# Kernel tuning notes

Measured on AMD Instinct MI355X. Metric: run time of the kernel, lower is better.

The kernel has to match this reference:

```python
import jax, jax.numpy as jnp
import numpy as np


def _ln(x, g, b, eps=1e-5):
    m = x.mean(-1, keepdims=True)
    v = x.var(-1, keepdims=True)
    return (x - m) / jnp.sqrt(v + eps) * g + b


def _causal_linear_attn(q, k, v, eps=1e-3):
    # q, k, v: (b, h, n, d). Matches lucidrains causal_linear_attn with bucket_size=1:
    # q -> softmax over feature dim, k -> exp, inclusive cumsum of k and k(outer)v over n.
    dh = q.shape[-1]
    q = jax.nn.softmax(q, axis=-1) * (dh ** -0.5)
    k = jnp.exp(k)
    k_cum = jnp.cumsum(k, axis=2)                                  # (b,h,n,d)
    ctx = jnp.cumsum(k[..., :, None] * v[..., None, :], axis=2)    # (b,h,n,d,d) running sum of k_i v_i^T
    d_inv = 1.0 / jnp.clip(jnp.einsum('bhnd,bhnd->bhn', k_cum, q), eps, None)
    return jnp.einsum('bhnd,bhnde->bhne', q, ctx) * d_inv[..., None]


def reference(x, ln1_g, ln1_b, Wq, Wk, Wv, Wo, bo, ln2_g, ln2_b, W1, b1, W2, b2, n_heads):
    depth = Wq.shape[0]
    B, N, D = x.shape
    H = int(n_heads)
    dh = D // H
    for i in range(depth):
        # --- pre-norm linear self-attention block ---
        xn = _ln(x, ln1_g[i], ln1_b[i])
        q = (xn @ Wq[i]).reshape(B, N, H, dh).transpose(0, 2, 1, 3)
        k = (xn @ Wk[i]).reshape(B, N, H, dh).transpose(0, 2, 1, 3)
        v = (xn @ Wv[i]).reshape(B, N, H, dh).transpose(0, 2, 1, 3)
        a = _causal_linear_attn(q, k, v)
        a = a.transpose(0, 2, 1, 3).reshape(B, N, D)
        x = x + a @ Wo[i] + bo[i]
        # --- pre-norm feed-forward block (mult=4, exact GELU) ---
        xn = _ln(x, ln2_g[i], ln2_b[i])
        x = x + jax.nn.gelu(xn @ W1[i] + b1[i], approximate=False) @ W2[i] + b2[i]
    return x


def setup_inputs() -> dict:
    key = jax.random.key(0)
    ks = jax.random.split(key, 8)
    B, N, D, H, depth = 2, 2048, 1024, 16, 2
    FF = 4 * D
    s = D ** -0.5
    x = jax.random.normal(ks[0], (B, N, D), dtype=jnp.float32)
    Wq = jax.random.normal(ks[1], (depth, D, D), dtype=jnp.float32) * s
    Wk = jax.random.normal(ks[2], (depth, D, D), dtype=jnp.float32) * s
    Wv = jax.random.normal(ks[3], (depth, D, D), dtype=jnp.float32) * s
    Wo = jax.random.normal(ks[4], (depth, D, D), dtype=jnp.float32) * s
    W1 = jax.random.normal(ks[5], (depth, D, FF), dtype=jnp.float32) * s
    W2 = jax.random.normal(ks[6], (depth, FF, D), dtype=jnp.float32) * (FF ** -0.5)
    return dict(
        x=x,
        ln1_g=jnp.ones((depth, D), jnp.float32), ln1_b=jnp.zeros((depth, D), jnp.float32),
        Wq=Wq, Wk=Wk, Wv=Wv, Wo=Wo, bo=jnp.zeros((depth, D), jnp.float32),
        ln2_g=jnp.ones((depth, D), jnp.float32), ln2_b=jnp.zeros((depth, D), jnp.float32),
        W1=W1, b1=jnp.zeros((depth, FF), jnp.float32),
        W2=W2, b2=jnp.zeros((depth, D), jnp.float32),
        n_heads=H,
    )
```

## Files before the change

kernel.cpp:

```cpp
#include <hip/hip_runtime.h>
#include <cmath>

#define BB 2
#define SEQ 2048
#define DIM 1024
#define NH 16
#define DH 64
#define DEPTH 2
#define FFD 4096
#define CHK 64
#define NCHK (SEQ/CHK)
#define ROWS (BB*SEQ)
#define QKP (3*DIM)

typedef __bf16 bf16x8 __attribute__((ext_vector_type(8)));
typedef __bf16 bf16x4 __attribute__((ext_vector_type(4)));
typedef float  f32x4  __attribute__((ext_vector_type(4)));

#define AS1 __attribute__((address_space(1)))
#define AS3 __attribute__((address_space(3)))
#define FENCE() asm volatile("" ::: "memory")

__device__ __forceinline__ float gelu_fast(float x) {
    float x3 = x * x * x;
    float y = 1.5957691216057308f * (x + 0.044715f * x3);
    return x * __builtin_amdgcn_rcpf(1.0f + __expf(-y));
}

__device__ __forceinline__ int swz128(int row, int col) {
    return row * 64 + (col ^ ((row & 7) << 3));
}

__device__ __forceinline__ void swz_tile(int bid, int NX, int NY, int& tx, int& ty) {
    int NB = NX * NY;
    int q = NB >> 3, r = NB & 7;
    int xcd = bid & 7, seq = bid >> 3;
    int start = (xcd < r) ? xcd * (q + 1) : r * (q + 1) + (xcd - r) * q;
    int wgid = start + seq;
    int g = 0, rem = wgid;
    int gw = (NX < 4) ? NX : 4;
    while (rem >= gw * NY) {
        rem -= gw * NY; g++;
        int left = NX - 4 * g;
        gw = left < 4 ? left : 4;
    }
    ty = rem / gw;
    tx = 4 * g + rem % gw;
}

__global__ __launch_bounds__(256) void ln_kernel(
    const float* __restrict__ x, const float* __restrict__ g,
    const float* __restrict__ b, __bf16* __restrict__ out)
{
    int row = blockIdx.x;
    const float4* xr = (const float4*)(x + (size_t)row * DIM);
    int t = threadIdx.x;
    float4 v = xr[t];
    float s  = v.x + v.y + v.z + v.w;
    float ss = v.x*v.x + v.y*v.y + v.z*v.z + v.w*v.w;
    #pragma unroll
    for (int off = 32; off > 0; off >>= 1) {
        s  += __shfl_down(s, off);
        ss += __shfl_down(ss, off);
    }
    __shared__ float wsum[4], wsq[4], stats[2];
    int wid = t >> 6, lane = t & 63;
    if (lane == 0) { wsum[wid] = s; wsq[wid] = ss; }
    __syncthreads();
    if (t == 0) {
        float S  = wsum[0] + wsum[1] + wsum[2] + wsum[3];
        float SS = wsq[0] + wsq[1] + wsq[2] + wsq[3];
        float mean = S * (1.0f / DIM);
        float var  = SS * (1.0f / DIM) - mean * mean;
        stats[0] = mean;
        stats[1] = rsqrtf(var + 1e-5f);
    }
    __syncthreads();
    float mean = stats[0], rstd = stats[1];
    float4 gv = ((const float4*)g)[t];
    float4 bv = ((const float4*)b)[t];
    bf16x4 o;
    o[0] = (__bf16)((v.x - mean) * rstd * gv.x + bv.x);
    o[1] = (__bf16)((v.y - mean) * rstd * gv.y + bv.y);
    o[2] = (__bf16)((v.z - mean) * rstd * gv.z + bv.z);
    o[3] = (__bf16)((v.w - mean) * rstd * gv.w + bv.w);
    *(bf16x4*)(out + (size_t)row * DIM + t * 4) = o;
}

__global__ __launch_bounds__(256) void transpose_all(
    const float* __restrict__ wq, const float* __restrict__ wk,
    const float* __restrict__ wv, const float* __restrict__ wo,
    const float* __restrict__ w1, const float* __restrict__ w2,
    __bf16* __restrict__ wqkt, __bf16* __restrict__ wot,
    __bf16* __restrict__ w1t, __bf16* __restrict__ w2t)
{
    int id = blockIdx.x;
    const float* W; __bf16* Wt; int K, N, txt, tyt;
    if (id < 4096) {
        int seg = id >> 10, r = id & 1023;
        K = DIM; N = DIM;
        txt = r & 31; tyt = r >> 5;
        W  = seg == 0 ? wq : seg == 1 ? wk : seg == 2 ? wv : wo;
        Wt = seg < 3 ? wqkt + (size_t)seg * DIM * DIM : wot;
    } else if (id < 8192) {
        int r = id - 4096;
        K = DIM; N = FFD;
        txt = r & 127; tyt = r >> 7;
        W = w1; Wt = w1t;
    } else {
        int r = id - 8192;
        K = FFD; N = DIM;
        txt = r & 31; tyt = r >> 5;
        W = w2; Wt = w2t;
    }
    __shared__ float tile[32][33];
    int bx = txt * 32, by = tyt * 32;
    int tx = threadIdx.x & 31, ty = threadIdx.x >> 5;
    #pragma unroll
    for (int i = 0; i < 32; i += 8)
        tile[ty + i][tx] = W[(size_t)(by + ty + i) * N + bx + tx];
    __syncthreads();
    #pragma unroll
    for (int i = 0; i < 32; i += 8)
        Wt[(size_t)(bx + ty + i) * K + by + tx] = (__bf16)tile[tx][ty + i];
}

__global__ __launch_bounds__(256) void transpose_v(
    const __bf16* __restrict__ qkv, __bf16* __restrict__ vT)
{
    __shared__ __bf16 tile[64 * 64];
    int bx = blockIdx.x;
    int by = blockIdx.y;
    int t = threadIdx.x;
    int r0 = t >> 3, sl = t & 7;
    #pragma unroll
    for (int i = 0; i < 2; i++) {
        int row = i * 32 + r0;
        bf16x8 d = *(const bf16x8*)(qkv + (size_t)(bx * 64 + row) * QKP + 2 * DIM + by * 64 + sl * 8);
        *(bf16x8*)&tile[row * 64 + ((sl ^ (row & 7)) << 3)] = d;
    }
    __syncthreads();
    #pragma unroll
    for (int i = 0; i < 2; i++) {
        int d = i * 32 + r0;
        int rbase = sl * 8;
        bf16x8 o;
        #pragma unroll
        for (int j = 0; j < 8; j++) {
            int rr = rbase + j;
            o[j] = tile[rr * 64 + (((((d >> 3)) ^ (rr & 7)) << 3) | (d & 7))];
        }
        *(bf16x8*)(vT + (size_t)(by * 64 + d) * ROWS + bx * 64 + rbase) = o;
    }
}

#define TBM 256
#define TBK 64
template<int MODE, int OUTBF, int NBF>
__global__ __launch_bounds__(512) void gemm256(
    const __bf16* __restrict__ A, const __bf16* __restrict__ Bt,
    void* __restrict__ Cv, const float* __restrict__ bias,
    const float* __restrict__ res, int M, int N, int K, int Kp,
    int NXT, int NYT, int NS)
{
    constexpr int ASZ = TBM * TBK;
    constexpr int BSZ = NBF * 64 * TBK;
    __shared__ __bf16 lds[2 * (ASZ + BSZ)];
    int nb = NXT * NYT;
    int sk = blockIdx.x / nb;
    int tx, ty;
    swz_tile(blockIdx.x % nb, NXT, NYT, tx, ty);
    if (NS > 1) {
        A  += (size_t)sk * K;
        Bt += (size_t)sk * K;
        Cv = (void*)((char*)Cv + (size_t)sk * M * N * (OUTBF ? 2 : 4));
    }
    const int bm = ty * TBM, bn = tx * (NBF * 64);
    const int t = threadIdx.x;
    const int l = t & 63, w = t >> 6;
    const int wm = w >> 2, wn = w & 3;
    const int lm = l & 15, lk = l >> 4;

    f32x4 acc[8][NBF] = {};
    const int nt = K / TBK;
    const int NIT = nt / 2;

    auto Aoff = [&](int bf) { return bf * (ASZ + BSZ); };
    auto Boff = [&](int bf) { return bf * (ASZ + BSZ) + ASZ; };

    const int s7 = lm & 7;
    const int c0 = (lk ^ s7) << 3;
    const int c1 = ((4 ^ lk) ^ s7) << 3;
    const __bf16* pA[2][2] = {
        { &lds[Aoff(0) + (wm * 128 + lm) * 64 + c0], &lds[Aoff(0) + (wm * 128 + lm) * 64 + c1] },
        { &lds[Aoff(1) + (wm * 128 + lm) * 64 + c0], &lds[Aoff(1) + (wm * 128 + lm) * 64 + c1] } };
    const __bf16* pB[2][2] = {
        { &lds[Boff(0) + (wn * (NBF * 16) + lm) * 64 + c0], &lds[Boff(0) + (wn * (NBF * 16) + lm) * 64 + c1] },
        { &lds[Boff(1) + (wn * (NBF * 16) + lm) * 64 + c0], &lds[Boff(1) + (wn * (NBF * 16) + lm) * 64 + c1] } };

    const int srow0 = t >> 3;
    const int scol0 = ((t & 7) ^ (srow0 & 7)) * 8;
    const __bf16* gAb = A + (size_t)(bm + srow0) * Kp + scol0;
    const __bf16* gBb = Bt + (size_t)(bn + srow0) * Kp + scol0;
    const int ldsw = w * 512;

    auto STAGEA = [&](int bf, int kt) {
        #pragma unroll
        for (int u = 0; u < 4; u++)
            __builtin_amdgcn_global_load_lds(
                (const AS1 void*)(gAb + (size_t)(u * 64) * Kp + kt * 64),
                (AS3 void*)(&lds[Aoff(bf) + u * 4096 + ldsw]), 16, 0, 0);
    };
    auto STAGEB = [&](int bf, int kt) {
        #pragma unroll
        for (int u = 0; u < NBF; u++)
            __builtin_amdgcn_global_load_lds(
                (const AS1 void*)(gBb + (size_t)(u * 64) * Kp + kt * 64),
                (AS3 void*)(&lds[Boff(bf) + u * 4096 + ldsw]), 16, 0, 0);
    };
    auto VMCNT_N = [&]() {
        if constexpr (NBF == 4) asm volatile("s_waitcnt vmcnt(4)" ::: "memory");
        else if constexpr (NBF == 3) asm volatile("s_waitcnt vmcnt(3)" ::: "memory");
        else asm volatile("s_waitcnt vmcnt(2)" ::: "memory");
    };
    auto LDA = [&](int bf, int g, bf16x8* af) {
        #pragma unroll
        for (int j = 0; j < 4; j++) {
            af[j * 2 + 0] = *(const bf16x8*)(pA[bf][0] + (g * 4 + j) * 1024);
            af[j * 2 + 1] = *(const bf16x8*)(pA[bf][1] + (g * 4 + j) * 1024);
        }
    };
    auto LDB = [&](int bf, bf16x8* bfv) {
        #pragma unroll
        for (int n = 0; n < NBF; n++) {
            bfv[n * 2 + 0] = *(const bf16x8*)(pB[bf][0] + n * 1024);
            bfv[n * 2 + 1] = *(const bf16x8*)(pB[bf][1] + n * 1024);
        }
    };
    auto MM2 = [&](int g, bf16x8* af, bf16x8* bfv) {
        __builtin_amdgcn_s_setprio(1);
        #pragma unroll
        for (int j = 0; j < 4; j++)
            #pragma unroll
            for (int n = 0; n < NBF; n++)
                #pragma unroll
                for (int kk = 0; kk < 2; kk++)
                    acc[g * 4 + j][n] = __builtin_amdgcn_mfma_f32_16x16x32_bf16(
                        af[j * 2 + kk], bfv[n * 2 + kk], acc[g * 4 + j][n], 0, 0, 0);
        __builtin_amdgcn_s_setprio(0);
    };

    STAGEA(0, 0); STAGEB(0, 0); STAGEB(1, 1);
    VMCNT_N();
    __builtin_amdgcn_s_barrier();

    bf16x8 aF[8], aFn[8], bF[2 * NBF];
    for (int it = 0; it < NIT; it++) {
        int u = 2 * it + 1, T2 = 2 * it + 2, U2 = 2 * it + 3;
        LDA(0, 0, aF); LDB(0, bF);
        STAGEA(1, u);
        FENCE(); __builtin_amdgcn_s_barrier();
        LDA(0, 1, aFn);
        MM2(0, aF, bF);
        FENCE(); __builtin_amdgcn_s_barrier();
        if (T2 < nt) {
            STAGEB(0, T2);
            VMCNT_N();
        } else {
            asm volatile("s_waitcnt vmcnt(0)" ::: "memory");
        }
        __builtin_amdgcn_s_barrier();
        MM2(1, aFn, bF);
        FENCE(); __builtin_amdgcn_s_barrier();
        LDA(1, 0, aF); LDB(1, bF);
        if (T2 < nt) STAGEA(0, T2);
        FENCE(); __builtin_amdgcn_s_barrier();
        LDA(1, 1, aFn);
        MM2(0, aF, bF);
        FENCE(); __builtin_amdgcn_s_barrier();
        if (U2 < nt) {
            STAGEB(1, U2);
            VMCNT_N();
        } else {
            asm volatile("s_waitcnt vmcnt(0)" ::: "memory");
        }
        __builtin_amdgcn_s_barrier();
        MM2(1, aFn, bF);
        FENCE(); __builtin_amdgcn_s_barrier();
    }

    #pragma unroll
    for (int m = 0; m < 8; m++) {
        #pragma unroll
        for (int n = 0; n < NBF; n++) {
            int col = bn + wn * (NBF * 16) + n * 16 + lm;
            #pragma unroll
            for (int r = 0; r < 4; r++) {
                int row = bm + wm * 128 + m * 16 + lk * 4 + r;
                float v = acc[m][n][r];
                if (MODE == 1) v += res[(size_t)row * N + col] + bias[col];
                if (MODE == 2) v = gelu_fast(v + bias[col]);
                if (OUTBF) ((__bf16*)Cv)[(size_t)row * N + col] = (__bf16)v;
                else       ((float*)Cv)[(size_t)row * N + col] = v;
            }
        }
    }
}

template<int DOLN>
__global__ __launch_bounds__(256) void reduce4ln(
    const __bf16* __restrict__ parts, const float* __restrict__ bias,
    float* __restrict__ x, const float* __restrict__ g,
    const float* __restrict__ b, __bf16* __restrict__ xn)
{
    const size_t PS = (size_t)ROWS * DIM;
    int row = blockIdx.x, t = threadIdx.x;
    size_t base = (size_t)row * DIM + t * 4;
    float4 xr = *(const float4*)(x + base);
    float4 bv = ((const float4*)bias)[t];
    float o0 = xr.x + bv.x, o1 = xr.y + bv.y, o2 = xr.z + bv.z, o3 = xr.w + bv.w;
    #pragma unroll
    for (int s = 0; s < 4; s++) {
        bf16x4 p = *(const bf16x4*)(parts + s * PS + base);
        o0 += (float)p[0]; o1 += (float)p[1]; o2 += (float)p[2]; o3 += (float)p[3];
    }
    float4 o = {o0, o1, o2, o3};
    *(float4*)(x + base) = o;
    if constexpr (DOLN) {
        float s  = o0 + o1 + o2 + o3;
        float ss = o0*o0 + o1*o1 + o2*o2 + o3*o3;
        #pragma unroll
        for (int off = 32; off > 0; off >>= 1) {
            s  += __shfl_down(s, off);
            ss += __shfl_down(ss, off);
        }
        __shared__ float wsum[4], wsq[4], stats[2];
        int wid = t >> 6, lane = t & 63;
        if (lane == 0) { wsum[wid] = s; wsq[wid] = ss; }
        __syncthreads();
        if (t == 0) {
            float S  = wsum[0] + wsum[1] + wsum[2] + wsum[3];
            float SS = wsq[0] + wsq[1] + wsq[2] + wsq[3];
            float mean = S * (1.0f / DIM);
            float var  = SS * (1.0f / DIM) - mean * mean;
            stats[0] = mean;
            stats[1] = rsqrtf(var + 1e-5f);
        }
        __syncthreads();
        float mean = stats[0], rstd = stats[1];
        float4 gv = ((const float4*)g)[t];
        float4 bvv = ((const float4*)b)[t];
        bf16x4 on;
        on[0] = (__bf16)((o0 - mean) * rstd * gv.x + bvv.x);
        on[1] = (__bf16)((o1 - mean) * rstd * gv.y + bvv.y);
        on[2] = (__bf16)((o2 - mean) * rstd * gv.z + bvv.z);
        on[3] = (__bf16)((o3 - mean) * rstd * gv.w + bvv.w);
        *(bf16x4*)(xn + base) = on;
    }
}

__global__ __launch_bounds__(256) void attn_local_m(
    const __bf16* __restrict__ qkv, const __bf16* __restrict__ vTg,
    float* __restrict__ KVT, float* __restrict__ Ksum)
{
    int blk = blockIdx.x;
    int c = blk % NCHK, bh = blk / NCHK;
    int b = bh / NH, h = bh % NH;
    __shared__ __bf16 ek_s[64 * 64];
    __shared__ __bf16 ekT_s[64 * 68];
    __shared__ float ksum_p[4][64];
    int t = threadIdx.x, w = t >> 6, l = t & 63;
    size_t rowbase = (size_t)(b * SEQ + c * CHK);

    {
        int m = t >> 2, dq = t & 3;
        const __bf16* kr = qkv + (rowbase + m) * QKP + DIM + h * DH + dq * 16;
        bf16x8 k0 = *(const bf16x8*)kr;
        bf16x8 k1 = *(const bf16x8*)(kr + 8);
        bf16x8 e0, e1;
        #pragma unroll
        for (int j = 0; j < 8; j++) {
            e0[j] = (__bf16)__expf((float)k0[j]);
            e1[j] = (__bf16)__expf((float)k1[j]);
        }
        *(bf16x8*)&ek_s[swz128(m, dq * 16)] = e0;
        *(bf16x8*)&ek_s[swz128(m, dq * 16 + 8)] = e1;
    }
    __syncthreads();
    {
        float kacc = 0.f;
        #pragma unroll
        for (int g = 0; g < 4; g++) {
            bf16x4 pk;
            #pragma unroll
            for (int j = 0; j < 4; j++) {
                __bf16 e = ek_s[swz128(w * 16 + g * 4 + j, l)];
                pk[j] = e;
                kacc += (float)e;
            }
            *(bf16x4*)&ekT_s[l * 68 + w * 16 + g * 4] = pk;
        }
        ksum_p[w][l] = kacc;
    }
    __syncthreads();
    f32x4 acc[4] = {};
    const __bf16* vbase = vTg + (size_t)(h * DH + w * 16 + (l & 15)) * ROWS
                        + (size_t)b * SEQ + c * CHK + (l >> 4) * 8;
    bf16x8 a0 = *(const bf16x8*)vbase;
    bf16x8 a1 = *(const bf16x8*)(vbase + 32);
    #pragma unroll
    for (int fn = 0; fn < 4; fn++) {
        int rbase = (fn * 16 + (l & 15)) * 68 + (l >> 4) * 8;
        bf16x4 b0a = *(const bf16x4*)&ekT_s[rbase];
        bf16x4 b0b = *(const bf16x4*)&ekT_s[rbase + 4];
        bf16x4 b1a = *(const bf16x4*)&ekT_s[rbase + 32];
        bf16x4 b1b = *(const bf16x4*)&ekT_s[rbase + 36];
        bf16x8 b0, b1;
        #pragma unroll
        for (int j = 0; j < 4; j++) {
            b0[j] = b0a[j]; b0[j + 4] = b0b[j];
            b1[j] = b1a[j]; b1[j + 4] = b1b[j];
        }
        acc[fn] = __builtin_amdgcn_mfma_f32_16x16x32_bf16(a0, b0, acc[fn], 0, 0, 0);
        acc[fn] = __builtin_amdgcn_mfma_f32_16x16x32_bf16(a1, b1, acc[fn], 0, 0, 0);
    }
    float* kvout = KVT + (size_t)(bh * NCHK + c) * (DH * DH);
    #pragma unroll
    for (int fn = 0; fn < 4; fn++)
        #pragma unroll
        for (int r = 0; r < 4; r++)
            kvout[(w * 16 + (l >> 4) * 4 + r) * DH + fn * 16 + (l & 15)] = acc[fn][r];
    if (t < 64) {
        float s = ksum_p[0][t] + ksum_p[1][t] + ksum_p[2][t] + ksum_p[3][t];
        Ksum[(size_t)(bh * NCHK + c) * DH + t] = s;
    }
}

__global__ __launch_bounds__(256) void attn_scan2(
    float* __restrict__ KV, float* __restrict__ Ksum)
{
    int bh = blockIdx.y;
    int bx = blockIdx.x;
    int t = threadIdx.x;
    if (bx < 16) {
        int elem = bx * 256 + t;
        float run = 0.f;
        for (int c = 0; c < NCHK; c++) {
            float* p = KV + ((size_t)(bh * NCHK + c)) * (DH * DH) + elem;
            float tmp = *p;
            *p = run;
            run += tmp;
        }
    } else if (t < DH) {
        float run = 0.f;
        for (int c = 0; c < NCHK; c++) {
            float* p = Ksum + ((size_t)(bh * NCHK + c)) * DH + t;
            float tmp = *p;
            *p = run;
            run += tmp;
        }
    }
}

__global__ __launch_bounds__(256) void attn_out_m(
    const __bf16* __restrict__ qkv, const __bf16* __restrict__ vTg,
    const float* __restrict__ KVT, const float* __restrict__ Ksum,
    __bf16* __restrict__ ag)
{
    int blk = blockIdx.x;
    int c = blk % NCHK, bh = blk / NCHK;
    int b = bh / NH, h = bh % NH;
    __shared__ __bf16 q_s[64 * 64];
    __shared__ __bf16 ek_s[64 * 64];
    __shared__ __bf16 s_s[64 * 64];
    __shared__ __bf16 kvT_s[64 * 64];
    __shared__ float denom_s[64];
    int t = threadIdx.x, w = t >> 6, l = t & 63;
    size_t rowbase = (size_t)(b * SEQ + c * CHK);

    {
        int i = t >> 2, dq = t & 3;
        const __bf16* qr = qkv + (rowbase + i) * QKP + h * DH + dq * 16;
        bf16x8 q0 = *(const bf16x8*)qr, q1 = *(const bf16x8*)(qr + 8);
        float qf[16];
        #pragma unroll
        for (int j = 0; j < 8; j++) { qf[j] = (float)q0[j]; qf[8 + j] = (float)q1[j]; }
        float mx = qf[0];
        #pragma unroll
        for (int j = 1; j < 16; j++) mx = fmaxf(mx, qf[j]);
        mx = fmaxf(mx, __shfl_xor(mx, 1));
        mx = fmaxf(mx, __shfl_xor(mx, 2));
        float ss = 0.f;
        #pragma unroll
        for (int j = 0; j < 16; j++) { qf[j] = __expf(qf[j] - mx); ss += qf[j]; }
        ss += __shfl_xor(ss, 1);
        ss += __shfl_xor(ss, 2);
        float sc = 0.125f / ss;
        bf16x8 o0, o1;
        #pragma unroll
        for (int j = 0; j < 8; j++) {
            o0[j] = (__bf16)(qf[j] * sc);
            o1[j] = (__bf16)(qf[8 + j] * sc);
        }
        *(bf16x8*)&q_s[swz128(i, dq * 16)] = o0;
        *(bf16x8*)&q_s[swz128(i, dq * 16 + 8)] = o1;
        const float* kp = Ksum + (size_t)(bh * NCHK + c) * DH + dq * 16;
        float dk = 0.f;
        #pragma unroll
        for (int j = 0; j < 16; j++) dk += (qf[j] * sc) * kp[j];
        dk += __shfl_xor(dk, 1);
        dk += __shfl_xor(dk, 2);
        if (dq == 0) denom_s[i] = dk;
    }
    {
        int m = t >> 2, dq = t & 3;
        const __bf16* kr = qkv + (rowbase + m) * QKP + DIM + h * DH + dq * 16;
        bf16x8 k0 = *(const bf16x8*)kr, k1 = *(const bf16x8*)(kr + 8);
        bf16x8 e0, e1;
        #pragma unroll
        for (int j = 0; j < 8; j++) {
            e0[j] = (__bf16)__expf((float)k0[j]);
            e1[j] = (__bf16)__expf((float)k1[j]);
        }
        *(bf16x8*)&ek_s[swz128(m, dq * 16)] = e0;
        *(bf16x8*)&ek_s[swz128(m, dq * 16 + 8)] = e1;
    }
    {
        int e = t >> 2, dq = t & 3;
        const float* kvr = KVT + (size_t)(bh * NCHK + c) * (DH * DH) + e * DH + dq * 16;
        bf16x8 o0, o1;
        #pragma unroll
        for (int j = 0; j < 8; j++) { o0[j] = (__bf16)kvr[j]; o1[j] = (__bf16)kvr[8 + j]; }
        *(bf16x8*)&kvT_s[swz128(e, dq * 16)] = o0;
        *(bf16x8*)&kvT_s[swz128(e, dq * 16 + 8)] = o1;
    }
    __syncthreads();

    bf16x8 bq0 = *(const bf16x8*)&q_s[swz128(w * 16 + (l & 15), (l >> 4) * 8)];
    bf16x8 bq1 = *(const bf16x8*)&q_s[swz128(w * 16 + (l & 15), 32 + (l >> 4) * 8)];
    int i_col = w * 16 + (l & 15);
    float dsum = 0.f;
    #pragma unroll
    for (int fm = 0; fm < 4; fm++) {
        bf16x8 ae0 = *(const bf16x8*)&ek_s[swz128(fm * 16 + (l & 15), (l >> 4) * 8)];
        bf16x8 ae1 = *(const bf16x8*)&ek_s[swz128(fm * 16 + (l & 15), 32 + (l >> 4) * 8)];
        f32x4 z = {};
        z = __builtin_amdgcn_mfma_f32_16x16x32_bf16(ae0, bq0, z, 0, 0, 0);
        z = __builtin_amdgcn_mfma_f32_16x16x32_bf16(ae1, bq1, z, 0, 0, 0);
        bf16x4 pk;
        #pragma unroll
        for (int r = 0; r < 4; r++) {
            int m = fm * 16 + (l >> 4) * 4 + r;
            float v = (m <= i_col) ? z[r] : 0.f;
            pk[r] = (__bf16)v;
            dsum += (float)pk[r];
        }
        *(bf16x4*)&s_s[swz128(i_col, fm * 16 + (l >> 4) * 4)] = pk;
    }
    dsum += __shfl_xor(dsum, 16);
    dsum += __shfl_xor(dsum, 32);
    if (l < 16) denom_s[w * 16 + l] += dsum;

    bf16x8 as0 = *(const bf16x8*)&s_s[swz128(w * 16 + (l & 15), (l >> 4) * 8)];
    bf16x8 as1 = *(const bf16x8*)&s_s[swz128(w * 16 + (l & 15), 32 + (l >> 4) * 8)];
    f32x4 oacc[4] = {};
    #pragma unroll
    for (int fn = 0; fn < 4; fn++) {
        const __bf16* vb = vTg + (size_t)(h * DH + fn * 16 + (l & 15)) * ROWS
                         + (size_t)b * SEQ + c * CHK + (l >> 4) * 8;
        bf16x8 bv0 = *(const bf16x8*)vb;
        bf16x8 bv1 = *(const bf16x8*)(vb + 32);
        bf16x8 bk0 = *(const bf16x8*)&kvT_s[swz128(fn * 16 + (l & 15), (l >> 4) * 8)];
        bf16x8 bk1 = *(const bf16x8*)&kvT_s[swz128(fn * 16 + (l & 15), 32 + (l >> 4) * 8)];
        f32x4 z = oacc[fn];
        z = __builtin_amdgcn_mfma_f32_16x16x32_bf16(as0, bv0, z, 0, 0, 0);
        z = __builtin_amdgcn_mfma_f32_16x16x32_bf16(as1, bv1, z, 0, 0, 0);
        z = __builtin_amdgcn_mfma_f32_16x16x32_bf16(bq0, bk0, z, 0, 0, 0);
        z = __builtin_amdgcn_mfma_f32_16x16x32_bf16(bq1, bk1, z, 0, 0, 0);
        oacc[fn] = z;
    }
    #pragma unroll
    for (int r = 0; r < 4; r++) {
        int i = w * 16 + (l >> 4) * 4 + r;
        float dinv = 1.0f / fmaxf(denom_s[i], 1e-3f);
        #pragma unroll
        for (int fn = 0; fn < 4; fn++)
            ag[(rowbase + i) * DIM + h * DH + fn * 16 + (l & 15)] = (__bf16)(oacc[fn][r] * dinv);
    }
}

extern "C" void kernel_launch(void* const* d_in, const int* in_sizes, int n_in,
                              void* d_out, int out_size, void* d_ws, size_t ws_size,
                              hipStream_t stream) {
    (void)in_sizes; (void)n_in; (void)out_size; (void)ws_size;
    const float* x_in  = (const float*)d_in[0];
    const float* ln1_g = (const float*)d_in[1];
    const float* ln1_b = (const float*)d_in[2];
    const float* Wq    = (const float*)d_in[3];
    const float* Wk    = (const float*)d_in[4];
    const float* Wv    = (const float*)d_in[5];
    const float* Wo    = (const float*)d_in[6];
    const float* bo    = (const float*)d_in[7];
    const float* ln2_g = (const float*)d_in[8];
    const float* ln2_b = (const float*)d_in[9];
    const float* W1    = (const float*)d_in[10];
    const float* b1    = (const float*)d_in[11];
    const float* W2    = (const float*)d_in[12];
    const float* b2    = (const float*)d_in[13];

    float* x = (float*)d_out;
    const size_t MB = 1024 * 1024;
    char* base = (char*)d_ws;

    __bf16* qkv    = (__bf16*)base;
    __bf16* partsO = (__bf16*)base;
    __bf16* h1     = (__bf16*)base;
    __bf16* vTg    = (__bf16*)(base + 24 * MB);
    __bf16* xn     = (__bf16*)(base + 32 * MB);
    __bf16* parts  = (__bf16*)(base + 32 * MB);
    __bf16* a      = (__bf16*)(base + 40 * MB);
    float*  KVT    = (float*)(base + 48 * MB);
    float*  Ks     = (float*)(base + 64 * MB);
    __bf16* wqkt   = (__bf16*)(base + 65 * MB);
    __bf16* wot    = (__bf16*)(base + 71 * MB);
    __bf16* w1t    = (__bf16*)(base + 73 * MB);
    __bf16* w2t    = (__bf16*)(base + 81 * MB);

    const size_t SZ = (size_t)ROWS * DIM;
    hipMemcpyAsync(x, x_in, SZ * sizeof(float), hipMemcpyDeviceToDevice, stream);

    dim3 gScan(17, BB * NH);
    dim3 gTv(ROWS / 64, DIM / 64);

    for (int l = 0; l < DEPTH; l++) {
        const float* wq = Wq + (size_t)l * DIM * DIM;
        const float* wk = Wk + (size_t)l * DIM * DIM;
        const float* wv = Wv + (size_t)l * DIM * DIM;
        const float* wo = Wo + (size_t)l * DIM * DIM;
        const float* w1 = W1 + (size_t)l * DIM * FFD;
        const float* w2 = W2 + (size_t)l * FFD * DIM;

        transpose_all<<<12288, 256, 0, stream>>>(wq, wk, wv, wo, w1, w2,
                                                 wqkt, wot, w1t, w2t);

        if (l == 0)
            ln_kernel<<<ROWS, 256, 0, stream>>>(x, ln1_g, ln1_b, xn);
        gemm256<0, 1, 3><<<16 * 16, 512, 0, stream>>>(xn, wqkt, qkv, nullptr, nullptr,
                                                      ROWS, QKP, DIM, DIM, 16, 16, 1);
        transpose_v<<<gTv, 256, 0, stream>>>(qkv, vTg);
        attn_local_m<<<BB * NH * NCHK, 256, 0, stream>>>(qkv, vTg, KVT, Ks);
        attn_scan2<<<gScan, 256, 0, stream>>>(KVT, Ks);
        attn_out_m<<<BB * NH * NCHK, 256, 0, stream>>>(qkv, vTg, KVT, Ks, a);
        gemm256<0, 1, 4><<<4 * 16 * 4, 512, 0, stream>>>(a, wot, partsO, nullptr, nullptr,
                                                         ROWS, DIM, DIM / 4, DIM, 4, 16, 4);
        reduce4ln<1><<<ROWS, 256, 0, stream>>>(partsO, bo + l * DIM, x,
                                               ln2_g + l * DIM, ln2_b + l * DIM, xn);

        gemm256<2, 1, 4><<<16 * 16, 512, 0, stream>>>(xn, w1t, h1, b1 + l * FFD, nullptr,
                                                      ROWS, FFD, DIM, DIM, 16, 16, 1);
        gemm256<0, 1, 4><<<4 * 16 * 4, 512, 0, stream>>>(h1, w2t, parts, nullptr, nullptr,
                                                         ROWS, DIM, FFD / 4, FFD, 4, 16, 4);
        if (l + 1 < DEPTH)
            reduce4ln<1><<<ROWS, 256, 0, stream>>>(parts, b2 + l * DIM, x,
                                                   ln1_g + (l + 1) * DIM,
                                                   ln1_b + (l + 1) * DIM, xn);
        else
            reduce4ln<0><<<ROWS, 256, 0, stream>>>(parts, b2 + l * DIM, x,
                                                   nullptr, nullptr, nullptr);
    }
}
```

Baseline: 390.8 us.

## Split GEMM mainloop into quarter-tile phases with half-staged global loads

Restructures the 256-row GEMM main loop so each k-tile is computed in four quarter phases (A half × B half), with global-to-LDS staging split into halves interleaved between phases and explicit lgkmcnt/vmcnt waits. The aim is to cut register pressure from holding full A/B fragment sets and to spread memory traffic more evenly against MFMA work. In exchange it adds roughly twice as many barriers per iteration and fragile hand-tuned vmcnt counts that could stall or race if miscounted.

```diff
diff --git a/kernel.cpp b/kernel.cpp
--- a/kernel.cpp
+++ b/kernel.cpp
@@ -20,6 +20,15 @@
 #define AS1 __attribute__((address_space(1)))
 #define AS3 __attribute__((address_space(3)))
 #define FENCE() asm volatile("" ::: "memory")
+#define LGKM0() asm volatile("s_waitcnt lgkmcnt(0)" ::: "memory")
+
+template<int N> __device__ __forceinline__ void vmcnt_wait() {
+    if constexpr (N == 0) asm volatile("s_waitcnt vmcnt(0)" ::: "memory");
+    else if constexpr (N == 3) asm volatile("s_waitcnt vmcnt(3)" ::: "memory");
+    else if constexpr (N == 4) asm volatile("s_waitcnt vmcnt(4)" ::: "memory");
+    else if constexpr (N == 5) asm volatile("s_waitcnt vmcnt(5)" ::: "memory");
+    else asm volatile("s_waitcnt vmcnt(6)" ::: "memory");
+}
 
 __device__ __forceinline__ float gelu_fast(float x) {
     float x3 = x * x * x;
@@ -165,6 +174,8 @@
 {
     constexpr int ASZ = TBM * TBK;
     constexpr int BSZ = NBF * 64 * TBK;
+    constexpr int VM4 = (NBF == 4) ? 4 : 3;
+    constexpr int VM8 = (NBF == 4) ? 6 : 5;
     __shared__ __bf16 lds[2 * (ASZ + BSZ)];
     int nb = NXT * NYT;
     int sk = blockIdx.x / nb;
@@ -204,88 +215,134 @@
     const __bf16* gBb = Bt + (size_t)(bn + srow0) * Kp + scol0;
     const int ldsw = w * 512;
 
-    auto STAGEA = [&](int bf, int kt) {
-        #pragma unroll
-        for (int u = 0; u < 4; u++)
+    auto STAGEA_H = [&](int bf, int hf, int kt) {
+        #pragma unroll
+        for (int i = 0; i < 2; i++) {
+            int u = hf * 2 + i;
             __builtin_amdgcn_global_load_lds(
                 (const AS1 void*)(gAb + (size_t)(u * 64) * Kp + kt * 64),
                 (AS3 void*)(&lds[Aoff(bf) + u * 4096 + ldsw]), 16, 0, 0);
+        }
     };
-    auto STAGEB = [&](int bf, int kt) {
-        #pragma unroll
-        for (int u = 0; u < NBF; u++)
-            __builtin_amdgcn_global_load_lds(
-                (const AS1 void*)(gBb + (size_t)(u * 64) * Kp + kt * 64),
-                (AS3 void*)(&lds[Boff(bf) + u * 4096 + ldsw]), 16, 0, 0);
+    auto STAGEB_H = [&](int bf, int hf, int kt) {
+        const int cnt = (NBF == 4) ? 2 : (hf == 0 ? 2 : 1);
+        const int u0  = (NBF == 4) ? hf * 2 : (hf == 0 ? 0 : 2);
+        #pragma unroll
+        for (int i = 0; i < 2; i++) {
+            if (i < cnt) {
+                int u = u0 + i;
+                __builtin_amdgcn_global_load_lds(
+                    (const AS1 void*)(gBb + (size_t)(u * 64) * Kp + kt * 64),
+                    (AS3 void*)(&lds[Boff(bf) + u * 4096 + ldsw]), 16, 0, 0);
+            }
+        }
     };
-    auto VMCNT_N = [&]() {
-        if constexpr (NBF == 4) asm volatile("s_waitcnt vmcnt(4)" ::: "memory");
-        else if constexpr (NBF == 3) asm volatile("s_waitcnt vmcnt(3)" ::: "memory");
-        else asm volatile("s_waitcnt vmcnt(2)" ::: "memory");
+    auto LDA = [&](int bf, int g, bf16x8* aH) {
+        #pragma unroll
+        for (int j = 0; j < 4; j++) {
+            aH[j * 2 + 0] = *(const bf16x8*)(pA[bf][0] + (g * 4 + j) * 1024);
+            aH[j * 2 + 1] = *(const bf16x8*)(pA[bf][1] + (g * 4 + j) * 1024);
+        }
     };
-    auto LDA = [&](int bf, int g, bf16x8* af) {
-        #pragma unroll
-        for (int j = 0; j < 4; j++) {
-            af[j * 2 + 0] = *(const bf16x8*)(pA[bf][0] + (g * 4 + j) * 1024);
-            af[j * 2 + 1] = *(const bf16x8*)(pA[bf][1] + (g * 4 + j) * 1024);
+    auto LDB0 = [&](int bf, bf16x8* b0) {
+        #pragma unroll
+        for (int n = 0; n < 2; n++) {
+            b0[n * 2 + 0] = *(const bf16x8*)(pB[bf][0] + n * 1024);
+            b0[n * 2 + 1] = *(const bf16x8*)(pB[bf][1] + n * 1024);
         }
     };
-    auto LDB = [&](int bf, bf16x8* bfv) {
-        #pragma unroll
-        for (int n = 0; n < NBF; n++) {
-            bfv[n * 2 + 0] = *(const bf16x8*)(pB[bf][0] + n * 1024);
-            bfv[n * 2 + 1] = *(const bf16x8*)(pB[bf][1] + n * 1024);
+    auto LDB1 = [&](int bf, bf16x8* b1) {
+        #pragma unroll
+        for (int n = 0; n < NBF - 2; n++) {
+            b1[n * 2 + 0] = *(const bf16x8*)(pB[bf][0] + (2 + n) * 1024);
+            b1[n * 2 + 1] = *(const bf16x8*)(pB[bf][1] + (2 + n) * 1024);
         }
     };
-    auto MM2 = [&](int g, bf16x8* af, bf16x8* bfv) {
+    auto MMQ0 = [&](int g, bf16x8* aH, bf16x8* b0) {
         __builtin_amdgcn_s_setprio(1);
         #pragma unroll
         for (int j = 0; j < 4; j++)
             #pragma unroll
-            for (int n = 0; n < NBF; n++)
+            for (int nn = 0; nn < 2; nn++)
                 #pragma unroll
                 for (int kk = 0; kk < 2; kk++)
-                    acc[g * 4 + j][n] = __builtin_amdgcn_mfma_f32_16x16x32_bf16(
-                        af[j * 2 + kk], bfv[n * 2 + kk], acc[g * 4 + j][n], 0, 0, 0);
+                    acc[g * 4 + j][nn] = __builtin_amdgcn_mfma_f32_16x16x32_bf16(
+                        aH[j * 2 + kk], b0[nn * 2 + kk], acc[g * 4 + j][nn], 0, 0, 0);
         __builtin_amdgcn_s_setprio(0);
     };
-
-    STAGEA(0, 0); STAGEB(0, 0); STAGEB(1, 1);
-    VMCNT_N();
+    auto MMQ1 = [&](int g, bf16x8* aH, bf16x8* b1) {
+        __builtin_amdgcn_s_setprio(1);
+        #pragma unroll
+        for (int j = 0; j < 4; j++)
+            #pragma unroll
+            for (int nn = 0; nn < NBF - 2; nn++)
+                #pragma unroll
+                for (int kk = 0; kk < 2; kk++)
+                    acc[g * 4 + j][2 + nn] = __builtin_amdgcn_mfma_f32_16x16x32_bf16(
+                        aH[j * 2 + kk], b1[nn * 2 + kk], acc[g * 4 + j][2 + nn], 0, 0, 0);
+        __builtin_amdgcn_s_setprio(0);
+    };
+
+    STAGEA_H(0, 0, 0); STAGEA_H(0, 1, 0); STAGEB_H(0, 0, 0); STAGEB_H(0, 1, 0);
+    STAGEB_H(1, 0, 1); STAGEB_H(1, 1, 1); STAGEA_H(1, 0, 1);
+    vmcnt_wait<VM8>();
     __builtin_amdgcn_s_barrier();
 
-    bf16x8 aF[8], aFn[8], bF[2 * NBF];
+    bf16x8 aH[8], bH0[4], bH1[2 * (NBF - 2)];
     for (int it = 0; it < NIT; it++) {
         int u = 2 * it + 1, T2 = 2 * it + 2, U2 = 2 * it + 3;
-        LDA(0, 0, aF); LDB(0, bF);
-        STAGEA(1, u);
-        FENCE(); __builtin_amdgcn_s_barrier();
-        LDA(0, 1, aFn);
-        MM2(0, aF, bF);
+        LDA(0, 0, aH); LDB0(0, bH0);
+        STAGEA_H(1, 1, u);
+        FENCE(); __builtin_amdgcn_s_barrier();
+        LGKM0();
+        MMQ0(0, aH, bH0);
+        FENCE(); __builtin_amdgcn_s_barrier();
+        LDB1(0, bH1);
+        FENCE(); __builtin_amdgcn_s_barrier();
+        LGKM0();
+        MMQ1(0, aH, bH1);
+        FENCE(); __builtin_amdgcn_s_barrier();
+        LDA(0, 1, aH);
+        if (T2 < nt) STAGEB_H(0, 0, T2);
+        FENCE(); __builtin_amdgcn_s_barrier();
+        LGKM0();
+        MMQ1(1, aH, bH1);
         FENCE(); __builtin_amdgcn_s_barrier();
         if (T2 < nt) {
-            STAGEB(0, T2);
-            VMCNT_N();
+            STAGEB_H(0, 1, T2);
+            vmcnt_wait<VM4>();
         } else {
-            asm volatile("s_waitcnt vmcnt(0)" ::: "memory");
+            vmcnt_wait<0>();
         }
         __builtin_amdgcn_s_barrier();
-        MM2(1, aFn, bF);
-        FENCE(); __builtin_amdgcn_s_barrier();
-        LDA(1, 0, aF); LDB(1, bF);
-        if (T2 < nt) STAGEA(0, T2);
-        FENCE(); __builtin_amdgcn_s_barrier();
-        LDA(1, 1, aFn);
-        MM2(0, aF, bF);
+        MMQ0(1, aH, bH0);
+        FENCE(); __builtin_amdgcn_s_barrier();
+        LDA(1, 0, aH); LDB0(1, bH0);
+        if (T2 < nt) STAGEA_H(0, 0, T2);
+        FENCE(); __builtin_amdgcn_s_barrier();
+        LGKM0();
+        MMQ0(0, aH, bH0);
+        FENCE(); __builtin_amdgcn_s_barrier();
+        LDB1(1, bH1);
+        if (T2 < nt) STAGEA_H(0, 1, T2);
+        FENCE(); __builtin_amdgcn_s_barrier();
+        LGKM0();
+        MMQ1(0, aH, bH1);
+        FENCE(); __builtin_amdgcn_s_barrier();
+        LDA(1, 1, aH);
+        if (U2 < nt) { STAGEB_H(1, 0, U2); STAGEB_H(1, 1, U2); }
+        FENCE(); __builtin_amdgcn_s_barrier();
+        LGKM0();
+        MMQ1(1, aH, bH1);
         FENCE(); __builtin_amdgcn_s_barrier();
         if (U2 < nt) {
-            STAGEB(1, U2);
-            VMCNT_N();
+            STAGEA_H(1, 0, U2);
+            vmcnt_wait<VM8>();
         } else {
-            asm volatile("s_waitcnt vmcnt(0)" ::: "memory");
+            vmcnt_wait<0>();
         }
         __builtin_amdgcn_s_barrier();
-        MM2(1, aFn, bF);
+        MMQ0(1, aH, bH0);
         FENCE(); __builtin_amdgcn_s_barrier();
     }
 
```

After: 390.5 us. No clear change (-0.1%).
